# Performance work log

Measured on AMD Instinct MI355X. Metric: run time of the kernel, lower is better.

Reference implementation:

```python
import jax, jax.numpy as jnp
import numpy as np

N_TOKENS = 16384
MODEL_DIM = 2048
NUM_EXPERTS = 64
K = 2


def setup_inputs() -> dict:
    key = jax.random.key(0)
    k1, k2 = jax.random.split(key)
    inputs = jax.random.normal(k1, (N_TOKENS, MODEL_DIM), dtype=jnp.float32)
    # gate weight, torch Linear(model_dim, num_experts, bias=False) -> [E, D]
    wg_weight = jax.random.normal(k2, (NUM_EXPERTS, MODEL_DIM), dtype=jnp.float32) * 0.02
    return {"inputs": inputs, "wg_weight": wg_weight}


def reference(inputs, wg_weight):
    E = wg_weight.shape[0]
    # gate computed in fp32 (module casts input and keeps wg in float32)
    logits = jnp.einsum("nd,ed->ne", inputs.astype(jnp.float32), wg_weight)
    probs = jax.nn.softmax(logits, axis=-1)                      # [N, E]
    topk_probs, topk_indices = jax.lax.top_k(probs, K)           # [N, K]
    flat_idx = topk_indices.reshape(-1)                          # [N*K]
    # stable sort of expert ids over all (token, slot) pairs
    sort_ordering = jnp.argsort(flat_idx)                        # [N*K]
    # reverse permutation: reversed[sort_ordering[i]] = i
    ar = jnp.arange(flat_idx.shape[0], dtype=sort_ordering.dtype)
    reversed_ordering = jnp.zeros_like(sort_ordering).at[sort_ordering].set(ar)
    # map slot index back to token index
    token_order = sort_ordering // K
    # per-expert counts (== unique_consecutive counts scattered into [E])
    input_splits = jnp.bincount(flat_idx, length=E).astype(jnp.int64)
    # combine weights: renormalize top-k probs via softmax when k > 1
    if K > 1:
        combine_weights = jax.nn.softmax(topk_probs, axis=-1)
    else:
        combine_weights = topk_probs
    combine_weights = combine_weights.reshape(-1).astype(inputs.dtype)
    return token_order, reversed_ordering, combine_weights, input_splits, probs
```

## Files before the change

### kernel.cpp

```cpp
#include <hip/hip_runtime.h>
#include <math.h>

#define N_TOKENS    16384
#define MODEL_DIM   2048
#define NUM_EXPERTS 64
#define NK          (N_TOKENS * 2)

#define OFF_TOKEN_ORDER 0
#define OFF_REVERSED    (NK)
#define OFF_COMBINE     (2 * NK)
#define OFF_SPLITS      (3 * NK)
#define OFF_PROBS       (3 * NK + NUM_EXPERTS)

#define BT 64
#define BK 64
#define NSEG 256
#define LSTRIDE 65

__global__ __launch_bounds__(256) void gate_partial(
    const float* __restrict__ x,
    const float* __restrict__ w,
    float* __restrict__ partials,
    int S, int kslice)
{
    __shared__ float a_tile[BT * 64];
    __shared__ float b_tile[NUM_EXPERTS * BK];

    const int tid = threadIdx.x;
    const int tb = blockIdx.x;
    const int sp = blockIdx.y;
    const int t0 = tb * BT;
    const int kbase = sp * kslice;
    const int tx = tid & 15;
    const int ty = tid >> 4;
    const int lk = tid & 15;
    const int lrow = tid >> 4;

    double accd[4][4];
#pragma unroll
    for (int i = 0; i < 4; i++)
#pragma unroll
        for (int j = 0; j < 4; j++) accd[i][j] = 0.0;

    for (int k0 = kbase; k0 < kbase + kslice; k0 += BK) {
#pragma unroll
        for (int j = 0; j < 4; j++) {
            const int row = lrow + j * 16;
            const int sc = ((lk + (row >> 2)) & 15) * 4;
            const float4 va = *(const float4*)(x + (size_t)(t0 + row) * MODEL_DIM + k0 + lk * 4);
            *(float4*)(a_tile + row * 64 + sc) = va;
            const float4 vb = *(const float4*)(w + (size_t)row * MODEL_DIM + k0 + lk * 4);
            *(float4*)(b_tile + row * 64 + sc) = vb;
        }
        __syncthreads();

        float accf[4][4];
#pragma unroll
        for (int i = 0; i < 4; i++)
#pragma unroll
            for (int j = 0; j < 4; j++) accf[i][j] = 0.0f;

#pragma unroll 4
        for (int k4 = 0; k4 < 16; k4++) {
            const int ca = ((k4 + ty) & 15) * 4;
            const int cb = ((k4 + tx) & 15) * 4;
            float4 a[4], b[4];
#pragma unroll
            for (int i = 0; i < 4; i++) a[i] = *(const float4*)(a_tile + (ty * 4 + i) * 64 + ca);
#pragma unroll
            for (int j = 0; j < 4; j++) b[j] = *(const float4*)(b_tile + (tx * 4 + j) * 64 + cb);
#pragma unroll
            for (int i = 0; i < 4; i++)
#pragma unroll
                for (int j = 0; j < 4; j++) {
                    accf[i][j] += a[i].x * b[j].x;
                    accf[i][j] += a[i].y * b[j].y;
                    accf[i][j] += a[i].z * b[j].z;
                    accf[i][j] += a[i].w * b[j].w;
                }
        }
#pragma unroll
        for (int i = 0; i < 4; i++)
#pragma unroll
            for (int j = 0; j < 4; j++) accd[i][j] += (double)accf[i][j];
        __syncthreads();
    }

    float* dst = partials + ((size_t)tb * S + sp) * 4096;
#pragma unroll
    for (int i = 0; i < 4; i++) {
        float4 v;
        v.x = (float)accd[i][0]; v.y = (float)accd[i][1];
        v.z = (float)accd[i][2]; v.w = (float)accd[i][3];
        *(float4*)(dst + (ty * 4 + i) * 64 + tx * 4) = v;
    }
}

__global__ __launch_bounds__(256) void reduce_kernel(
    const float* __restrict__ partials,
    float* __restrict__ out,
    int* __restrict__ flat_idx,
    int* __restrict__ segHist,
    int S)
{
    __shared__ float l_lds[BT * LSTRIDE];
    __shared__ float inv_lds[BT];
    __shared__ int hist[NUM_EXPERTS];

    const int tid = threadIdx.x;
    const int tb = blockIdx.x;
    const int t0 = tb * BT;
    const float* src = partials + (size_t)tb * S * 4096;

#pragma unroll
    for (int v = 0; v < 4; v++) {
        const int q = tid + v * 256;
        double a0 = 0.0, a1 = 0.0, a2 = 0.0, a3 = 0.0;
        for (int s = 0; s < S; s++) {
            const float4 p = *(const float4*)(src + (size_t)s * 4096 + q * 4);
            a0 += (double)p.x; a1 += (double)p.y; a2 += (double)p.z; a3 += (double)p.w;
        }
        const int f = q * 4;
        const int t = f >> 6;
        const int e = f & 63;
        float* row = l_lds + t * LSTRIDE + e;
        row[0] = (float)a0; row[1] = (float)a1; row[2] = (float)a2; row[3] = (float)a3;
    }
    if (tid < NUM_EXPERTS) hist[tid] = 0;
    __syncthreads();

    if (tid < BT) {
        const int t = tid;
        float* row = l_lds + t * LSTRIDE;
        float m = -INFINITY;
#pragma unroll
        for (int e = 0; e < NUM_EXPERTS; e++) m = fmaxf(m, row[e]);
        float l1 = -INFINITY, l2 = -INFINITY;
        int i1 = 0, i2 = 0;
        double s = 0.0;
        for (int e = 0; e < NUM_EXPERTS; e++) {
            const float l = row[e];
            if (l > l1) { l2 = l1; i2 = i1; l1 = l; i1 = e; }
            else if (l > l2) { l2 = l; i2 = e; }
            const float ex = expf(l - m);
            s += (double)ex;
            row[e] = ex;
        }
        const float inv = (float)(1.0 / s);
        inv_lds[t] = inv;
        const float p1 = expf(l1 - m) * inv;
        const float p2 = expf(l2 - m) * inv;
        const float e2 = expf(p2 - p1);
        const float r = 1.0f / (1.0f + e2);
        const int gtok = t0 + t;
        out[OFF_COMBINE + 2 * gtok]     = r;
        out[OFF_COMBINE + 2 * gtok + 1] = e2 * r;
        flat_idx[2 * gtok]     = i1;
        flat_idx[2 * gtok + 1] = i2;
        atomicAdd(&hist[i1], 1);
        atomicAdd(&hist[i2], 1);
    }
    __syncthreads();

    if (tid < NUM_EXPERTS) segHist[tb * NUM_EXPERTS + tid] = hist[tid];

#pragma unroll
    for (int r4 = 0; r4 < 4; r4++) {
        const int f = r4 * 1024 + tid * 4;
        const int t = f >> 6;
        const int e = f & 63;
        const float inv = inv_lds[t];
        float4 v;
        v.x = l_lds[t * LSTRIDE + e + 0] * inv;
        v.y = l_lds[t * LSTRIDE + e + 1] * inv;
        v.z = l_lds[t * LSTRIDE + e + 2] * inv;
        v.w = l_lds[t * LSTRIDE + e + 3] * inv;
        *(float4*)(out + OFF_PROBS + (size_t)(t0 + t) * NUM_EXPERTS + e) = v;
    }
}

__global__ __launch_bounds__(256) void scan_kernel(
    const int* __restrict__ segHist, int* __restrict__ segOff,
    float* __restrict__ out)
{
    __shared__ int h[NSEG * NUM_EXPERTS];
    __shared__ int gtot[4 * NUM_EXPERTS];
    __shared__ int base[NUM_EXPERTS];
    const int tid = threadIdx.x;
    for (int i = tid; i < NSEG * NUM_EXPERTS / 4; i += 256)
        *(int4*)(h + i * 4) = *(const int4*)(segHist + i * 4);
    __syncthreads();

    const int e = tid & 63;
    const int g = tid >> 6;
    int run = 0;
    for (int s = g * 64; s < g * 64 + 64; s++) {
        const int idx = s * NUM_EXPERTS + e;
        const int v = h[idx];
        h[idx] = run;
        run += v;
    }
    gtot[g * NUM_EXPERTS + e] = run;
    __syncthreads();

    if (tid < NUM_EXPERTS) {
        int b = 0;
#pragma unroll
        for (int gg = 0; gg < 4; gg++) {
            const int t = gtot[gg * NUM_EXPERTS + tid];
            gtot[gg * NUM_EXPERTS + tid] = b;
            b += t;
        }
        out[OFF_SPLITS + tid] = (float)b;
        int xs = b;
#pragma unroll
        for (int off = 1; off < 64; off <<= 1) {
            const int v = __shfl_up(xs, off);
            if (tid >= off) xs += v;
        }
        base[tid] = xs - b;
    }
    __syncthreads();

    const int myoff = gtot[g * NUM_EXPERTS + e] + base[e];
    for (int s = g * 64; s < g * 64 + 64; s++) {
        const int idx = s * NUM_EXPERTS + e;
        segOff[idx] = h[idx] + myoff;
    }
}

__global__ __launch_bounds__(256) void scatter_kernel(
    const int* __restrict__ flat_idx, const int* __restrict__ segOff,
    float* __restrict__ out)
{
    __shared__ int cnt[2 * NUM_EXPERTS];
    const int tid = threadIdx.x;
    const int i = blockIdx.x * 256 + tid;
    const int e = flat_idx[i];
    const int lane = tid & 63;
    const int wv = tid >> 6;
    const int segslot = wv >> 1;
    const int seg = i >> 7;

    if (tid < 2 * NUM_EXPERTS) cnt[tid] = 0;
    __syncthreads();

    unsigned long long match = ~0ull;
#pragma unroll
    for (int b = 0; b < 6; b++) {
        const unsigned long long m = __ballot((e >> b) & 1);
        match &= ((e >> b) & 1) ? m : ~m;
    }
    const int rank = __popcll(match & ((1ull << lane) - 1ull));

    int pos = 0;
    if ((wv & 1) == 0) {
        pos = segOff[seg * NUM_EXPERTS + e] + rank;
        if (lane == __builtin_ctzll(match))
            cnt[segslot * NUM_EXPERTS + e] = __popcll(match);
    }
    __syncthreads();
    if ((wv & 1) == 1)
        pos = segOff[seg * NUM_EXPERTS + e] + cnt[segslot * NUM_EXPERTS + e] + rank;

    out[OFF_TOKEN_ORDER + pos] = (float)(i >> 1);
    out[OFF_REVERSED + i]      = (float)pos;
}

extern "C" void kernel_launch(void* const* d_in, const int* in_sizes, int n_in,
                              void* d_out, int out_size, void* d_ws, size_t ws_size,
                              hipStream_t stream) {
    const float* x = (const float*)d_in[0];
    const float* w = (const float*)d_in[1];
    float* out = (float*)d_out;

    int* flat_idx = (int*)d_ws;
    int* segHist  = flat_idx + NK;
    int* segOff   = segHist + NSEG * NUM_EXPERTS;
    float* ws_part = (float*)(segOff + NSEG * NUM_EXPERTS);

    const size_t fixed_bytes = ((size_t)NK + 2 * NSEG * NUM_EXPERTS) * 4;
    const size_t avail = ws_size > fixed_bytes ? ws_size - fixed_bytes : 0;
    const size_t part1 = (size_t)N_TOKENS * NUM_EXPERTS * 4;

    int S;
    float* partials = ws_part;
    if      (avail >= 8 * part1) S = 8;
    else if (avail >= 4 * part1) S = 4;
    else if (avail >= 2 * part1) S = 2;
    else if (avail >= 1 * part1) S = 1;
    else { S = 1; partials = out + OFF_PROBS; }
    const int kslice = MODEL_DIM / S;

    gate_partial<<<dim3(N_TOKENS / BT, S), 256, 0, stream>>>(x, w, partials, S, kslice);
    reduce_kernel<<<NSEG, 256, 0, stream>>>(partials, out, flat_idx, segHist, S);
    scan_kernel<<<1, 256, 0, stream>>>(segHist, segOff, out);
    scatter_kernel<<<NK / 256, 256, 0, stream>>>(flat_idx, segOff, out);
}
```

Measured before the change: 245.6 us.

## Replace FP32 SIMT gate GEMM with split-FP16 MFMA fused with softmax/top-k

Result: no change. 245.2 us (-0.2%).

```diff
diff --git a/kernel.cpp b/kernel.cpp
--- a/kernel.cpp
+++ b/kernel.cpp
@@ -12,170 +12,211 @@
 #define OFF_SPLITS      (3 * NK)
 #define OFF_PROBS       (3 * NK + NUM_EXPERTS)
 
-#define BT 64
-#define BK 64
 #define NSEG 256
-#define LSTRIDE 65
-
-__global__ __launch_bounds__(256) void gate_partial(
-    const float* __restrict__ x,
-    const float* __restrict__ w,
-    float* __restrict__ partials,
-    int S, int kslice)
+#define NFRAG 16384
+
+typedef _Float16 half8 __attribute__((ext_vector_type(8)));
+typedef float    f32x4 __attribute__((ext_vector_type(4)));
+
+#define IMIN(a, b) ((a) < (b) ? (a) : (b))
+
+__global__ __launch_bounds__(256) void preconvert(
+    const float* __restrict__ w, half8* __restrict__ WH, half8* __restrict__ WL,
+    int* __restrict__ segHist)
 {
-    __shared__ float a_tile[BT * 64];
-    __shared__ float b_tile[NUM_EXPERTS * BK];
+    const int fr = blockIdx.x * 256 + threadIdx.x;
+    const int lane = fr & 63;
+    const int tile = (fr >> 6) & 3;
+    const int kstep = fr >> 8;
+    const int e = tile * 16 + (lane & 15);
+    const int kb = kstep * 32 + (lane >> 4) * 8;
+    const float* src = w + (size_t)e * MODEL_DIM + kb;
+    const float4 w0 = *(const float4*)(src);
+    const float4 w1 = *(const float4*)(src + 4);
+    const float av[8] = {w0.x, w0.y, w0.z, w0.w, w1.x, w1.y, w1.z, w1.w};
+    half8 hh, hl;
+#pragma unroll
+    for (int j = 0; j < 8; j++) {
+        const float v = av[j] * 64.0f;
+        const _Float16 h = (_Float16)v;
+        hh[j] = h;
+        hl[j] = (_Float16)((v - (float)h) * 4096.0f);
+    }
+    WH[fr] = hh;
+    WL[fr] = hl;
+    segHist[fr] = 0;
+}
+
+
+#define LOADB(BH_, BL_, G_) do {                                            \
+    const size_t bb_ = (size_t)(G_) * 256 + lane;                           \
+    _Pragma("unroll")                                                       \
+    for (int t_ = 0; t_ < 4; t_++) {                                        \
+        BH_[t_] = WH[bb_ + t_ * 64];                                        \
+        BL_[t_] = WL[bb_ + t_ * 64];                                        \
+    }                                                                       \
+} while (0)
+
+#define LOADA(DST_, KOFF_) do {                                             \
+    const int ko_ = (KOFF_);                                                \
+    _Pragma("unroll")                                                       \
+    for (int s_ = 0; s_ < 4; s_++) {                                        \
+        DST_[2*s_]   = *(const float4*)(px + ko_ + s_*32);                  \
+        DST_[2*s_+1] = *(const float4*)(px + ko_ + s_*32 + 4);              \
+    }                                                                       \
+} while (0)
+
+#define STEP(AV_, SI_, BHC_, BLC_, BHN_, BLN_, GN_) do {                    \
+    LOADB(BHN_, BLN_, GN_);                                                 \
+    const float4 A0_ = AV_[2*(SI_)];                                        \
+    const float4 A1_ = AV_[2*(SI_)+1];                                      \
+    const float av_[8] = {A0_.x,A0_.y,A0_.z,A0_.w,A1_.x,A1_.y,A1_.z,A1_.w}; \
+    half8 ah_, al_;                                                         \
+    _Pragma("unroll")                                                       \
+    for (int j_ = 0; j_ < 8; j_++) {                                        \
+        const float v_ = av_[j_];                                           \
+        const _Float16 h_ = (_Float16)v_;                                   \
+        ah_[j_] = h_;                                                       \
+        al_[j_] = (_Float16)((v_ - (float)h_) * 4096.0f);                   \
+    }                                                                       \
+    _Pragma("unroll")                                                       \
+    for (int t_ = 0; t_ < 4; t_++) {                                        \
+        accH[t_] = __builtin_amdgcn_mfma_f32_16x16x32_f16(ah_, BHC_[t_], accH[t_], 0, 0, 0); \
+        accC[t_] = __builtin_amdgcn_mfma_f32_16x16x32_f16(ah_, BLC_[t_], accC[t_], 0, 0, 0); \
+        accC[t_] = __builtin_amdgcn_mfma_f32_16x16x32_f16(al_, BHC_[t_], accC[t_], 0, 0, 0); \
+    }                                                                       \
+} while (0)
+
+__global__ __launch_bounds__(128, 2) void gate_fused(
+    const float* __restrict__ x, const half8* __restrict__ WH,
+    const half8* __restrict__ WL, float* __restrict__ out,
+    int* __restrict__ flat_idx, int* __restrict__ segHist)
+{
+    __shared__ double lds_d[64 * 17];
 
     const int tid = threadIdx.x;
-    const int tb = blockIdx.x;
-    const int sp = blockIdx.y;
-    const int t0 = tb * BT;
-    const int kbase = sp * kslice;
-    const int tx = tid & 15;
-    const int ty = tid >> 4;
-    const int lk = tid & 15;
-    const int lrow = tid >> 4;
-
-    double accd[4][4];
-#pragma unroll
-    for (int i = 0; i < 4; i++)
-#pragma unroll
-        for (int j = 0; j < 4; j++) accd[i][j] = 0.0;
-
-    for (int k0 = kbase; k0 < kbase + kslice; k0 += BK) {
-#pragma unroll
-        for (int j = 0; j < 4; j++) {
-            const int row = lrow + j * 16;
-            const int sc = ((lk + (row >> 2)) & 15) * 4;
-            const float4 va = *(const float4*)(x + (size_t)(t0 + row) * MODEL_DIM + k0 + lk * 4);
-            *(float4*)(a_tile + row * 64 + sc) = va;
-            const float4 vb = *(const float4*)(w + (size_t)row * MODEL_DIM + k0 + lk * 4);
-            *(float4*)(b_tile + row * 64 + sc) = vb;
-        }
-        __syncthreads();
-
-        float accf[4][4];
-#pragma unroll
-        for (int i = 0; i < 4; i++)
-#pragma unroll
-            for (int j = 0; j < 4; j++) accf[i][j] = 0.0f;
-
-#pragma unroll 4
-        for (int k4 = 0; k4 < 16; k4++) {
-            const int ca = ((k4 + ty) & 15) * 4;
-            const int cb = ((k4 + tx) & 15) * 4;
-            float4 a[4], b[4];
-#pragma unroll
-            for (int i = 0; i < 4; i++) a[i] = *(const float4*)(a_tile + (ty * 4 + i) * 64 + ca);
-#pragma unroll
-            for (int j = 0; j < 4; j++) b[j] = *(const float4*)(b_tile + (tx * 4 + j) * 64 + cb);
-#pragma unroll
-            for (int i = 0; i < 4; i++)
-#pragma unroll
-                for (int j = 0; j < 4; j++) {
-                    accf[i][j] += a[i].x * b[j].x;
-                    accf[i][j] += a[i].y * b[j].y;
-                    accf[i][j] += a[i].z * b[j].z;
-                    accf[i][j] += a[i].w * b[j].w;
-                }
-        }
-#pragma unroll
-        for (int i = 0; i < 4; i++)
-#pragma unroll
-            for (int j = 0; j < 4; j++) accd[i][j] += (double)accf[i][j];
-        __syncthreads();
-    }
-
-    float* dst = partials + ((size_t)tb * S + sp) * 4096;
-#pragma unroll
-    for (int i = 0; i < 4; i++) {
-        float4 v;
-        v.x = (float)accd[i][0]; v.y = (float)accd[i][1];
-        v.z = (float)accd[i][2]; v.w = (float)accd[i][3];
-        *(float4*)(dst + (ty * 4 + i) * 64 + tx * 4) = v;
-    }
-}
-
-__global__ __launch_bounds__(256) void reduce_kernel(
-    const float* __restrict__ partials,
-    float* __restrict__ out,
-    int* __restrict__ flat_idx,
-    int* __restrict__ segHist,
-    int S)
-{
-    __shared__ float l_lds[BT * LSTRIDE];
-    __shared__ float inv_lds[BT];
-    __shared__ int hist[NUM_EXPERTS];
-
-    const int tid = threadIdx.x;
-    const int tb = blockIdx.x;
-    const int t0 = tb * BT;
-    const float* src = partials + (size_t)tb * S * 4096;
-
-#pragma unroll
-    for (int v = 0; v < 4; v++) {
-        const int q = tid + v * 256;
-        double a0 = 0.0, a1 = 0.0, a2 = 0.0, a3 = 0.0;
-        for (int s = 0; s < S; s++) {
-            const float4 p = *(const float4*)(src + (size_t)s * 4096 + q * 4);
-            a0 += (double)p.x; a1 += (double)p.y; a2 += (double)p.z; a3 += (double)p.w;
-        }
-        const int f = q * 4;
-        const int t = f >> 6;
-        const int e = f & 63;
-        float* row = l_lds + t * LSTRIDE + e;
-        row[0] = (float)a0; row[1] = (float)a1; row[2] = (float)a2; row[3] = (float)a3;
-    }
-    if (tid < NUM_EXPERTS) hist[tid] = 0;
-    __syncthreads();
-
-    if (tid < BT) {
-        const int t = tid;
-        float* row = l_lds + t * LSTRIDE;
-        float m = -INFINITY;
-#pragma unroll
-        for (int e = 0; e < NUM_EXPERTS; e++) m = fmaxf(m, row[e]);
+    const int wv = tid >> 6;
+    const int lane = tid & 63;
+    const int t0 = blockIdx.x * 16;
+    const int col = lane & 15;
+    const int kg = lane >> 4;
+
+    const float* px = x + (size_t)(t0 + col) * MODEL_DIM + wv * 1024 + kg * 8;
+    const int gbase = wv * 32;
+
+    f32x4 accH[4], accC[4];
+    double accD[4][4];
+#pragma unroll
+    for (int t = 0; t < 4; t++) {
+        accH[t] = (f32x4){0.f, 0.f, 0.f, 0.f};
+        accC[t] = (f32x4){0.f, 0.f, 0.f, 0.f};
+#pragma unroll
+        for (int r = 0; r < 4; r++) accD[t][r] = 0.0;
+    }
+
+    float4 aA[8], aB[8];
+    half8 bh0[4], bl0[4], bh1[4], bl1[4];
+
+    LOADA(aA, 0);
+    LOADB(bh0, bl0, gbase);
+
+    for (int it = 0; it < 4; it++) {
+        const int ss = it * 2;
+        const int gb = gbase + it * 8;
+        LOADA(aB, (ss + 1) * 128);
+        STEP(aA, 0, bh0, bl0, bh1, bl1, IMIN(gb + 1, 63));
+        STEP(aA, 1, bh1, bl1, bh0, bl0, IMIN(gb + 2, 63));
+        STEP(aA, 2, bh0, bl0, bh1, bl1, IMIN(gb + 3, 63));
+        STEP(aA, 3, bh1, bl1, bh0, bl0, IMIN(gb + 4, 63));
+        LOADA(aA, IMIN(ss + 2, 7) * 128);
+        STEP(aB, 0, bh0, bl0, bh1, bl1, IMIN(gb + 5, 63));
+        STEP(aB, 1, bh1, bl1, bh0, bl0, IMIN(gb + 6, 63));
+        STEP(aB, 2, bh0, bl0, bh1, bl1, IMIN(gb + 7, 63));
+        STEP(aB, 3, bh1, bl1, bh0, bl0, IMIN(gb + 8, 63));
+#pragma unroll
+        for (int t = 0; t < 4; t++)
+#pragma unroll
+            for (int r = 0; r < 4; r++) {
+                accD[t][r] += (double)accH[t][r] + (double)accC[t][r] * (1.0 / 4096.0);
+                accH[t][r] = 0.0f;
+                accC[t][r] = 0.0f;
+            }
+    }
+
+    if (wv == 1) {
+#pragma unroll
+        for (int t = 0; t < 4; t++)
+#pragma unroll
+            for (int r = 0; r < 4; r++)
+                lds_d[lane * 17 + t * 4 + r] = accD[t][r];
+    }
+    __syncthreads();
+    if (wv == 1) return;
+
+#pragma unroll
+    for (int t = 0; t < 4; t++)
+#pragma unroll
+        for (int r = 0; r < 4; r++)
+            accD[t][r] += lds_d[lane * 17 + t * 4 + r];
+
+    const int rowg = lane >> 4;
+#pragma unroll
+    for (int r = 0; r < 4; r++) {
+        float lv[4];
+#pragma unroll
+        for (int t = 0; t < 4; t++) lv[t] = (float)(accD[t][r] * (1.0 / 64.0));
+
+        float m = fmaxf(fmaxf(lv[0], lv[1]), fmaxf(lv[2], lv[3]));
+#pragma unroll
+        for (int d = 1; d < 16; d <<= 1) m = fmaxf(m, __shfl_xor(m, d));
+
         float l1 = -INFINITY, l2 = -INFINITY;
         int i1 = 0, i2 = 0;
-        double s = 0.0;
-        for (int e = 0; e < NUM_EXPERTS; e++) {
-            const float l = row[e];
-            if (l > l1) { l2 = l1; i2 = i1; l1 = l; i1 = e; }
-            else if (l > l2) { l2 = l; i2 = e; }
-            const float ex = expf(l - m);
-            s += (double)ex;
-            row[e] = ex;
-        }
-        const float inv = (float)(1.0 / s);
-        inv_lds[t] = inv;
-        const float p1 = expf(l1 - m) * inv;
-        const float p2 = expf(l2 - m) * inv;
-        const float e2 = expf(p2 - p1);
-        const float r = 1.0f / (1.0f + e2);
-        const int gtok = t0 + t;
-        out[OFF_COMBINE + 2 * gtok]     = r;
-        out[OFF_COMBINE + 2 * gtok + 1] = e2 * r;
-        flat_idx[2 * gtok]     = i1;
-        flat_idx[2 * gtok + 1] = i2;
-        atomicAdd(&hist[i1], 1);
-        atomicAdd(&hist[i2], 1);
-    }
-    __syncthreads();
-
-    if (tid < NUM_EXPERTS) segHist[tb * NUM_EXPERTS + tid] = hist[tid];
-
-#pragma unroll
-    for (int r4 = 0; r4 < 4; r4++) {
-        const int f = r4 * 1024 + tid * 4;
-        const int t = f >> 6;
-        const int e = f & 63;
-        const float inv = inv_lds[t];
-        float4 v;
-        v.x = l_lds[t * LSTRIDE + e + 0] * inv;
-        v.y = l_lds[t * LSTRIDE + e + 1] * inv;
-        v.z = l_lds[t * LSTRIDE + e + 2] * inv;
-        v.w = l_lds[t * LSTRIDE + e + 3] * inv;
-        *(float4*)(out + OFF_PROBS + (size_t)(t0 + t) * NUM_EXPERTS + e) = v;
+#pragma unroll
+        for (int t = 0; t < 4; t++) {
+            const float l = lv[t];
+            const int e = t * 16 + col;
+            if (l > l1)      { l2 = l1; i2 = i1; l1 = l; i1 = e; }
+            else if (l > l2) { l2 = l;  i2 = e; }
+        }
+#pragma unroll
+        for (int d = 1; d < 16; d <<= 1) {
+            const float ol1 = __shfl_xor(l1, d), ol2 = __shfl_xor(l2, d);
+            const int   oi1 = __shfl_xor(i1, d), oi2 = __shfl_xor(i2, d);
+            if (ol1 > l1 || (ol1 == l1 && oi1 < i1)) {
+                if (l1 > ol2 || (l1 == ol2 && i1 < oi2)) { l2 = l1;  i2 = i1;  }
+                else                                     { l2 = ol2; i2 = oi2; }
+                l1 = ol1; i1 = oi1;
+            } else if (ol1 > l2 || (ol1 == l2 && oi1 < i2)) {
+                l2 = ol1; i2 = oi1;
+            }
+        }
+
+        float ex[4];
+        double sd = 0.0;
+#pragma unroll
+        for (int t = 0; t < 4; t++) { ex[t] = expf(lv[t] - m); sd += (double)ex[t]; }
+#pragma unroll
+        for (int d = 1; d < 16; d <<= 1) sd += __shfl_xor(sd, d);
+        const float inv = (float)(1.0 / sd);
+
+        const int tok = t0 + rowg * 4 + r;
+        float* pp = out + OFF_PROBS + (size_t)tok * NUM_EXPERTS + col;
+#pragma unroll
+        for (int t = 0; t < 4; t++) pp[t * 16] = ex[t] * inv;
+
+        if (col == 0) {
+            const float p1 = expf(l1 - m) * inv;
+            const float p2 = expf(l2 - m) * inv;
+            const float e2 = expf(p2 - p1);
+            const float rr = 1.0f / (1.0f + e2);
+            out[OFF_COMBINE + 2 * tok]     = rr;
+            out[OFF_COMBINE + 2 * tok + 1] = e2 * rr;
+            flat_idx[2 * tok]     = i1;
+            flat_idx[2 * tok + 1] = i2;
+            atomicAdd(&segHist[(tok >> 6) * NUM_EXPERTS + i1], 1);
+            atomicAdd(&segHist[(tok >> 6) * NUM_EXPERTS + i2], 1);
+        }
     }
 }
 
@@ -277,23 +318,11 @@
     int* flat_idx = (int*)d_ws;
     int* segHist  = flat_idx + NK;
     int* segOff   = segHist + NSEG * NUM_EXPERTS;
-    float* ws_part = (float*)(segOff + NSEG * NUM_EXPERTS);
-
-    const size_t fixed_bytes = ((size_t)NK + 2 * NSEG * NUM_EXPERTS) * 4;
-    const size_t avail = ws_size > fixed_bytes ? ws_size - fixed_bytes : 0;
-    const size_t part1 = (size_t)N_TOKENS * NUM_EXPERTS * 4;
-
-    int S;
-    float* partials = ws_part;
-    if      (avail >= 8 * part1) S = 8;
-    else if (avail >= 4 * part1) S = 4;
-    else if (avail >= 2 * part1) S = 2;
-    else if (avail >= 1 * part1) S = 1;
-    else { S = 1; partials = out + OFF_PROBS; }
-    const int kslice = MODEL_DIM / S;
-
-    gate_partial<<<dim3(N_TOKENS / BT, S), 256, 0, stream>>>(x, w, partials, S, kslice);
-    reduce_kernel<<<NSEG, 256, 0, stream>>>(partials, out, flat_idx, segHist, S);
+    half8* WH = (half8*)(segOff + NSEG * NUM_EXPERTS);
+    half8* WL = WH + NFRAG;
+
+    preconvert<<<64, 256, 0, stream>>>(w, WH, WL, segHist);
+    gate_fused<<<N_TOKENS / 16, 128, 0, stream>>>(x, WH, WL, out, flat_idx, segHist);
     scan_kernel<<<1, 256, 0, stream>>>(segHist, segOff, out);
     scatter_kernel<<<NK / 256, 256, 0, stream>>>(flat_idx, segOff, out);
 }
```
